# Kernel optimization log

Hardware: AMD Instinct MI355X
Metric: run time of the kernel (lower is better)

Reference implementation:

```python
import jax, jax.numpy as jnp
import numpy as np

# Config matching init_kwargs: 63 single-grapheme tokens + optional blank -> C = 64,
# trivial (identity) lexicon, ngram = 0 (no transition model), allow_repeats = True.
# Under this config the GTN composition (target chain o lexicon -> tokens graph ->
# alignments, intersected with linear emission graph, forward_score) is exactly the
# CTC forward algorithm over the extended label sequence z = [blank, y1, blank, ...,
# yL, blank], with the s-2 -> s skip allowed for ALL non-blank states (allow_repeats).

B, T, C, L = 128, 3000, 64, 128
NEG = -1e30  # effective -inf, safe in fp32


def setup_inputs() -> dict:
    key = jax.random.key(0)
    k1, k2 = jax.random.split(key)
    inputs = jax.random.normal(k1, (B, T, C), dtype=jnp.float32)  # raw logits
    # target token ids in [0, C-2]; blank = C-1 is never a target
    targets = jax.random.randint(k2, (B, L), 0, C - 1, dtype=jnp.int32)
    return {"inputs": inputs, "targets": targets}


def reference(inputs, targets):
    Bv, Tv, Cv = inputs.shape
    Lv = targets.shape[1]
    S = 2 * Lv + 1
    blank = Cv - 1
    # transitions is None -> module applies log_softmax to inputs
    logp = jax.nn.log_softmax(inputs, axis=2)  # [B, T, C]
    # extended label sequence: blanks at even positions, targets at odd positions
    z = jnp.full((Bv, S), blank, dtype=jnp.int32).at[:, 1::2].set(targets)  # [B, S]
    # per-frame emission scores for each extended state: [B, T, S] -> [T, B, S]
    em = jnp.take_along_axis(logp, jnp.broadcast_to(z[:, None, :], (Bv, Tv, S)), axis=2)
    em = jnp.transpose(em, (1, 0, 2))
    # skip transition (s-2 -> s) allowed for every non-blank (odd) state because
    # allow_repeats=True (no z[s] != z[s-2] restriction)
    skip_ok = (jnp.arange(S) % 2 == 1)  # [S]

    alpha0 = (jnp.full((Bv, S), NEG, dtype=jnp.float32)
              .at[:, 0].set(em[0, :, 0])
              .at[:, 1].set(em[0, :, 1]))

    def step(alpha, e_t):
        a1 = jnp.pad(alpha[:, :-1], ((0, 0), (1, 0)), constant_values=NEG)
        a2 = jnp.pad(alpha[:, :-2], ((0, 0), (2, 0)), constant_values=NEG)
        a2 = jnp.where(skip_ok[None, :], a2, NEG)
        new = e_t + jax.scipy.special.logsumexp(jnp.stack([alpha, a1, a2], axis=0), axis=0)
        return new, None

    alphaT, _ = jax.lax.scan(step, alpha0, em[1:])  # [B, S]
    # accepting states: last label (S-2) and trailing blank (S-1)
    ll = jax.scipy.special.logsumexp(alphaT[:, S - 2:S], axis=1)  # [B]
    # reduction='none' -> scales = 1; forward returns torch.mean over batch
    return jnp.mean(-ll)
```

## Files before the change

kernel.cpp:

```cpp
#include <hip/hip_runtime.h>
#include <stdint.h>

#define BB 128
#define TT 3000
#define CC 64
#define LL 128
#define NEGf (-1e30f)
#define LOG2E 1.4426950408889634f
#define LN2f 0.6931471805599453f
#define F 12
#define NCH 250
#define NBUF 5
#define NPH (NCH + 3)
#define LSE_BLOCKS 512

typedef float f32x2 __attribute__((ext_vector_type(2)));

__device__ __forceinline__ float fexp2(float x){ return __builtin_amdgcn_exp2f(x); }
__device__ __forceinline__ float flog2(float x){ return __builtin_amdgcn_logf(x); }
__device__ __forceinline__ float shr1_neg(float x){
    int r = __builtin_amdgcn_update_dpp(__float_as_int(NEGf), __float_as_int(x),
                                        0x138, 0xF, 0xF, false);
    return __int_as_float(r);
}
#define DPPMAXT(x,c) fmaxf((x),__int_as_float(__builtin_amdgcn_update_dpp(0,__float_as_int(x),(c),0xF,0xF,true)))
#define DPPADDT(x,c) ((x)+__int_as_float(__builtin_amdgcn_update_dpp(0,__float_as_int(x),(c),0xF,0xF,true)))
#define RED64(OP,x) { x=OP(x,0x111); x=OP(x,0x112); x=OP(x,0x114); x=OP(x,0x118); x=OP(x,0x142); x=OP(x,0x143); }

__global__ __launch_bounds__(512) void fused_kernel(const float* __restrict__ in,
                                                    const int* __restrict__ tgt,
                                                    float* __restrict__ lse,
                                                    float* __restrict__ ll2){
    __shared__ float emR[NBUF][F][132];
    __shared__ float bndR[5][3][F];
    __shared__ float laL[3008];
    __shared__ float lbL[3008];
    __shared__ float dmp[64];
    if (blockIdx.x < BB) {
        const int b = blockIdx.x;
        const int wave = threadIdx.x >> 6;
        const int lane = threadIdx.x & 63;
        const float* fb = in + (size_t)b * TT * CC;
        const uint32_t em_base  = (uint32_t)(uintptr_t)&emR[0][0][0];
        const uint32_t bnd_base = (uint32_t)(uintptr_t)&bndR[0][0][0];
        const uint32_t la_base  = (uint32_t)(uintptr_t)&laL[0];
        const uint32_t dmp_base = (uint32_t)(uintptr_t)&dmp[0];

        if (wave < 4) {
            const int w = wave;
            __builtin_amdgcn_s_setprio(1);
            if (w == 0) {
                float* bp = &bndR[0][0][0];
                if (lane < 3*F) bp[lane] = NEGf;
                if (lane < 3) bndR[lane+1][0][0] = NEGf;
                if (lane < 8) { laL[3000+lane] = NEGf; lbL[3000+lane] = 0.f; }
            }
            const bool odd = (lane & 1);
            const uint32_t em_off = odd ? (uint32_t)(32*w + (lane>>1))*4u : 512u;
            float aa = (w==0 && lane==0) ? 0.f : NEGf;
            __syncthreads();
            for (int ph = 0; ph < NPH; ++ph) {
                const int x = ph - w;
                if (x >= 0 && x < NCH) {
                    const uint32_t buf = (uint32_t)(x % NBUF);
                    const uint32_t ra  = em_base + buf*(F*132u*4u) + em_off;
                    const uint32_t xm3 = (uint32_t)(x % 3);
                    const uint32_t xp3 = (uint32_t)((x+1) % 3);
                    const uint32_t rb  = bnd_base + (uint32_t)w*144u + xm3*48u;
                    const uint32_t wbm = (lane==63) ? (bnd_base + (uint32_t)(w+1)*144u + xm3*48u)
                                                    : (dmp_base + (uint32_t)lane*4u);
                    const uint32_t wbl = (lane==63) ? (bnd_base + (uint32_t)(w+1)*144u + xp3*48u)
                                                    : (dmp_base + (uint32_t)lane*4u);
                    const uint32_t wl  = (w==3 && lane==63) ? (la_base + (uint32_t)(x*F)*4u)
                                                            : (dmp_base + (uint32_t)lane*4u);
                    float e0,e1,e2,b0,b1,b2;
                    asm volatile("ds_read_b32 %0, %1 offset:0"   : "=v"(e0) : "v"(ra));
                    asm volatile("ds_read_b32 %0, %1 offset:0"   : "=v"(b0) : "v"(rb));
                    asm volatile("ds_read_b32 %0, %1 offset:528" : "=v"(e1) : "v"(ra));
                    asm volatile("ds_read_b32 %0, %1 offset:4"   : "=v"(b1) : "v"(rb));
                    #pragma unroll
                    for (int j = 0; j < F; ++j) {
                        const int jn = (j+2 < F) ? (j+2) : (F-1);
                        asm volatile("ds_read_b32 %0, %1 offset:%2" : "=v"(e2) : "v"(ra), "n"(jn*528));
                        asm volatile("ds_read_b32 %0, %1 offset:%2" : "=v"(b2) : "v"(rb), "n"(jn*4));
                        if (j == 0)      asm volatile("s_waitcnt lgkmcnt(4)" ::: "memory");
                        else if (j == 1) asm volatile("s_waitcnt lgkmcnt(6)" ::: "memory");
                        else             asm volatile("s_waitcnt lgkmcnt(8)" ::: "memory");
                        __builtin_amdgcn_sched_barrier(0);
                        float p1 = shr1_neg(aa);
                        float p2 = shr1_neg(p1);
                        p1 = (lane==0) ? b0 : p1;
                        p2 = (lane==1) ? b0 : p2;
                        float z = odd ? p2 : NEGf;
                        float mx = fmaxf(fmaxf(aa,p1),z);
                        float md = __builtin_amdgcn_fmed3f(aa,p1,z);
                        float mn = fminf(fminf(aa,p1),z);
                        float e  = fexp2(md-mx) + fexp2(mn-mx);
                        float v  = __builtin_fmaf(e,0.5f,-0.5f);
                        float h  = __builtin_fmaf(v,0.2f,-0.25f);
                        h = __builtin_fmaf(v,h,0.33333333f);
                        h = __builtin_fmaf(v,h,-0.5f);
                        h = __builtin_fmaf(v,h,1.0f);
                        aa = __builtin_fmaf(v*h, LOG2E, mx+1.0f) + e0;
                        if (j < F-1) { asm volatile("ds_write_b32 %0, %1 offset:%2" :: "v"(wbm), "v"(aa), "n"((j+1)*4)); }
                        else         { asm volatile("ds_write_b32 %0, %1 offset:0"  :: "v"(wbl), "v"(aa)); }
                        asm volatile("ds_write_b32 %0, %1 offset:%2" :: "v"(wl), "v"(aa), "n"(j*4));
                        e0=e1; b0=b1; e1=e2; b1=b2;
                    }
                    asm volatile("s_waitcnt lgkmcnt(0)" ::: "memory");
                }
                __syncthreads();
            }
            __syncthreads();
            if (w == 0) {
                const int base = lane*47;
                float seg = 0.f;
                for (int k = 0; k < 47; ++k) seg += lbL[base+k];
                float inc = seg;
                #pragma unroll
                for (int d = 1; d < 64; d <<= 1) {
                    float t = __shfl_up(inc, d, 64);
                    if (lane >= d) inc += t;
                }
                float CBtot = __int_as_float(__builtin_amdgcn_readlane(__float_as_int(inc), 63));
                float ex = inc - seg;
                float cb = ex, gm = NEGf;
                for (int k = 0; k < 47; ++k) {
                    int idx = base+k;
                    cb += lbL[idx];
                    float g = laL[idx] + (CBtot - cb);
                    g = (idx == 2999) ? NEGf : g;
                    gm = fmaxf(gm, g);
                }
                RED64(DPPMAXT, gm);
                float gmax = __int_as_float(__builtin_amdgcn_readlane(__float_as_int(gm), 63));
                cb = ex; float se = 0.f;
                for (int k = 0; k < 47; ++k) {
                    int idx = base+k;
                    cb += lbL[idx];
                    float g = laL[idx] + (CBtot - cb);
                    g = (idx == 2999) ? NEGf : g;
                    se += fexp2(g - gmax);
                }
                RED64(DPPADDT, se);
                float S = __int_as_float(__builtin_amdgcn_readlane(__float_as_int(se), 63));
                float la256 = gmax + flog2(S);
                float la255f = laL[2999];
                float m = fmaxf(la255f, la256);
                float r = m + flog2(1.0f + fexp2(-fabsf(la255f - la256)));
                if (lane == 0) ll2[b] = r;
            }
        } else {
            const int p = wave - 4;
            const int t0 = tgt[b*LL + 2*lane];
            const int t1 = tgt[b*LL + 2*lane + 1];
            auto produce = [&](int cc) {
                const int buf = cc % NBUF;
                const float* cbase = fb + (size_t)cc * F * CC;
                float v0[3], v1[3], vb[3];
                #pragma unroll
                for (int k = 0; k < 3; ++k) {
                    const float* fr = cbase + (3*p + k)*CC;
                    v0[k] = fr[t0]; v1[k] = fr[t1]; vb[k] = fr[63];
                }
                #pragma unroll
                for (int k = 0; k < 3; ++k) {
                    const int f = 3*p + k;
                    f32x2 wv; wv.x = v0[k]*LOG2E; wv.y = v1[k]*LOG2E;
                    *(f32x2*)&emR[buf][f][2*lane] = wv;
                    if (lane == 0) {
                        float xb = vb[k]*LOG2E;
                        emR[buf][f][128] = xb;
                        lbL[cc*F + f] = xb;
                    }
                }
            };
            produce(0);
            __syncthreads();
            for (int ph = 0; ph < NPH; ++ph) {
                if (ph + 1 < NCH) produce(ph + 1);
                __syncthreads();
            }
            __syncthreads();
        }
        return;
    }
    int wv = (blockIdx.x - BB) * 8 + (threadIdx.x >> 6);
    int lane = threadIdx.x & 63;
    const int stride = LSE_BLOCKS * 8;
    for (int row = wv; row < BB * TT; row += stride) {
        float x = in[(size_t)row * CC + lane];
        float m = x;
        #pragma unroll
        for (int d = 32; d >= 1; d >>= 1) m = fmaxf(m, __shfl_xor(m, d, 64));
        float s = fexp2((x - m) * LOG2E);
        #pragma unroll
        for (int d = 32; d >= 1; d >>= 1) s += __shfl_xor(s, d, 64);
        if (lane == 0) lse[row] = m + flog2(s) * LN2f;
    }
}

__global__ __launch_bounds__(256) void bsum_kernel(const float* __restrict__ lse,
                                                   const float* __restrict__ ll2,
                                                   float* __restrict__ lossb) {
    __shared__ float red[256];
    int b = blockIdx.x;
    float s = 0.f;
    for (int i = threadIdx.x; i < TT; i += 256) s += lse[(size_t)b * TT + i];
    red[threadIdx.x] = s;
    __syncthreads();
    #pragma unroll
    for (int w = 128; w >= 1; w >>= 1) {
        if (threadIdx.x < w) red[threadIdx.x] += red[threadIdx.x + w];
        __syncthreads();
    }
    if (threadIdx.x == 0) lossb[b] = red[0] - ll2[b] * LN2f;
}

__global__ __launch_bounds__(64) void final_kernel(const float* __restrict__ lossb,
                                                   float* __restrict__ out) {
    int lane = threadIdx.x;
    float v = lossb[lane] + lossb[lane + 64];
    #pragma unroll
    for (int d = 32; d >= 1; d >>= 1) v += __shfl_xor(v, d, 64);
    if (lane == 0) out[0] = v / (float)BB;
}

extern "C" void kernel_launch(void* const* d_in, const int* in_sizes, int n_in,
                              void* d_out, int out_size, void* d_ws, size_t ws_size,
                              hipStream_t stream) {
    const float* in = (const float*)d_in[0];
    const int* tg = (const int*)d_in[1];
    float* out = (float*)d_out;
    float* lse = (float*)d_ws;
    float* ll2 = lse + (size_t)BB * TT;
    float* lossb = ll2 + BB;

    hipLaunchKernelGGL(fused_kernel, dim3(BB + LSE_BLOCKS), dim3(512), 0, stream,
                       in, tg, lse, ll2);
    hipLaunchKernelGGL(bsum_kernel, dim3(BB), dim3(256), 0, stream, lse, ll2, lossb);
    hipLaunchKernelGGL(final_kernel, dim3(1), dim3(64), 0, stream, lossb, out);
}
```

Baseline: 291.6 us.

## Batch boundary reads, defer boundary writes, and prefetch producer loads a phase ahead

The recurrence waves now read all 12 boundary values with three ds_read_b128 up front instead of per-step scalar reads. Per-step dummy writes from every lane are replaced by storing a per-step history in registers, and only lane 63 writes the boundary and laL values after the chunk. The producer waves split global loads from LDS stores so loads for chunk ph+2 are issued before the barrier, hiding global latency across a phase. This aims to cut LDS traffic and wait stalls on the serial critical path, at the cost of more registers and a short write burst at the end of each chunk.

```diff
diff --git a/kernel.cpp b/kernel.cpp
--- a/kernel.cpp
+++ b/kernel.cpp
@@ -15,6 +15,7 @@
 #define LSE_BLOCKS 512
 
 typedef float f32x2 __attribute__((ext_vector_type(2)));
+typedef float f32x4 __attribute__((ext_vector_type(4)));
 
 __device__ __forceinline__ float fexp2(float x){ return __builtin_amdgcn_exp2f(x); }
 __device__ __forceinline__ float flog2(float x){ return __builtin_amdgcn_logf(x); }
@@ -32,10 +33,9 @@
                                                     float* __restrict__ lse,
                                                     float* __restrict__ ll2){
     __shared__ float emR[NBUF][F][132];
-    __shared__ float bndR[5][3][F];
+    __shared__ __align__(16) float bndR[4][3][F];
     __shared__ float laL[3008];
     __shared__ float lbL[3008];
-    __shared__ float dmp[64];
     if (blockIdx.x < BB) {
         const int b = blockIdx.x;
         const int wave = threadIdx.x >> 6;
@@ -43,16 +43,13 @@
         const float* fb = in + (size_t)b * TT * CC;
         const uint32_t em_base  = (uint32_t)(uintptr_t)&emR[0][0][0];
         const uint32_t bnd_base = (uint32_t)(uintptr_t)&bndR[0][0][0];
-        const uint32_t la_base  = (uint32_t)(uintptr_t)&laL[0];
-        const uint32_t dmp_base = (uint32_t)(uintptr_t)&dmp[0];
 
         if (wave < 4) {
             const int w = wave;
             __builtin_amdgcn_s_setprio(1);
             if (w == 0) {
-                float* bp = &bndR[0][0][0];
-                if (lane < 3*F) bp[lane] = NEGf;
-                if (lane < 3) bndR[lane+1][0][0] = NEGf;
+                if (lane < 36) (&bndR[0][0][0])[lane] = NEGf;
+                if (lane >= 1 && lane <= 3) bndR[lane][0][0] = NEGf;
                 if (lane < 8) { laL[3000+lane] = NEGf; lbL[3000+lane] = 0.f; }
             }
             const bool odd = (lane & 1);
@@ -67,30 +64,28 @@
                     const uint32_t xm3 = (uint32_t)(x % 3);
                     const uint32_t xp3 = (uint32_t)((x+1) % 3);
                     const uint32_t rb  = bnd_base + (uint32_t)w*144u + xm3*48u;
-                    const uint32_t wbm = (lane==63) ? (bnd_base + (uint32_t)(w+1)*144u + xm3*48u)
-                                                    : (dmp_base + (uint32_t)lane*4u);
-                    const uint32_t wbl = (lane==63) ? (bnd_base + (uint32_t)(w+1)*144u + xp3*48u)
-                                                    : (dmp_base + (uint32_t)lane*4u);
-                    const uint32_t wl  = (w==3 && lane==63) ? (la_base + (uint32_t)(x*F)*4u)
-                                                            : (dmp_base + (uint32_t)lane*4u);
-                    float e0,e1,e2,b0,b1,b2;
-                    asm volatile("ds_read_b32 %0, %1 offset:0"   : "=v"(e0) : "v"(ra));
-                    asm volatile("ds_read_b32 %0, %1 offset:0"   : "=v"(b0) : "v"(rb));
-                    asm volatile("ds_read_b32 %0, %1 offset:528" : "=v"(e1) : "v"(ra));
-                    asm volatile("ds_read_b32 %0, %1 offset:4"   : "=v"(b1) : "v"(rb));
+                    f32x4 B4a, B4b, B4c; float ef[F]; float hist[F];
+                    asm volatile("ds_read_b128 %0, %1 offset:0"  : "=v"(B4a) : "v"(rb));
+                    asm volatile("ds_read_b128 %0, %1 offset:16" : "=v"(B4b) : "v"(rb));
+                    asm volatile("ds_read_b128 %0, %1 offset:32" : "=v"(B4c) : "v"(rb));
+                    asm volatile("ds_read_b32 %0, %1 offset:0"    : "=v"(ef[0]) : "v"(ra));
+                    asm volatile("ds_read_b32 %0, %1 offset:528"  : "=v"(ef[1]) : "v"(ra));
+                    asm volatile("ds_read_b32 %0, %1 offset:1056" : "=v"(ef[2]) : "v"(ra));
                     #pragma unroll
                     for (int j = 0; j < F; ++j) {
-                        const int jn = (j+2 < F) ? (j+2) : (F-1);
-                        asm volatile("ds_read_b32 %0, %1 offset:%2" : "=v"(e2) : "v"(ra), "n"(jn*528));
-                        asm volatile("ds_read_b32 %0, %1 offset:%2" : "=v"(b2) : "v"(rb), "n"(jn*4));
-                        if (j == 0)      asm volatile("s_waitcnt lgkmcnt(4)" ::: "memory");
-                        else if (j == 1) asm volatile("s_waitcnt lgkmcnt(6)" ::: "memory");
-                        else             asm volatile("s_waitcnt lgkmcnt(8)" ::: "memory");
+                        if (j + 3 < F)
+                            asm volatile("ds_read_b32 %0, %1 offset:%2"
+                                         : "=v"(ef[j+3]) : "v"(ra), "n"((j+3)*528));
+                        if (j < F-3)       asm volatile("s_waitcnt lgkmcnt(3)" ::: "memory");
+                        else if (j == F-3) asm volatile("s_waitcnt lgkmcnt(2)" ::: "memory");
+                        else if (j == F-2) asm volatile("s_waitcnt lgkmcnt(1)" ::: "memory");
+                        else               asm volatile("s_waitcnt lgkmcnt(0)" ::: "memory");
                         __builtin_amdgcn_sched_barrier(0);
+                        float bj = (j < 4) ? B4a[j & 3] : ((j < 8) ? B4b[j & 3] : B4c[j & 3]);
                         float p1 = shr1_neg(aa);
                         float p2 = shr1_neg(p1);
-                        p1 = (lane==0) ? b0 : p1;
-                        p2 = (lane==1) ? b0 : p2;
+                        p1 = (lane==0) ? bj : p1;
+                        p2 = (lane==1) ? bj : p2;
                         float z = odd ? p2 : NEGf;
                         float mx = fmaxf(fmaxf(aa,p1),z);
                         float md = __builtin_amdgcn_fmed3f(aa,p1,z);
@@ -101,11 +96,18 @@
                         h = __builtin_fmaf(v,h,0.33333333f);
                         h = __builtin_fmaf(v,h,-0.5f);
                         h = __builtin_fmaf(v,h,1.0f);
-                        aa = __builtin_fmaf(v*h, LOG2E, mx+1.0f) + e0;
-                        if (j < F-1) { asm volatile("ds_write_b32 %0, %1 offset:%2" :: "v"(wbm), "v"(aa), "n"((j+1)*4)); }
-                        else         { asm volatile("ds_write_b32 %0, %1 offset:0"  :: "v"(wbl), "v"(aa)); }
-                        asm volatile("ds_write_b32 %0, %1 offset:%2" :: "v"(wl), "v"(aa), "n"(j*4));
-                        e0=e1; b0=b1; e1=e2; b1=b2;
+                        aa = __builtin_fmaf(v*h, LOG2E, mx+1.0f) + ef[j];
+                        hist[j] = aa;
+                    }
+                    if (w < 3 && lane == 63) {
+                        float* reg = &bndR[w+1][0][0];
+                        #pragma unroll
+                        for (int j = 0; j < F-1; ++j) reg[xm3*F + j + 1] = hist[j];
+                        reg[xp3*F + 0] = hist[F-1];
+                    }
+                    if (w == 3 && lane == 63) {
+                        #pragma unroll
+                        for (int j = 0; j < F; ++j) laL[x*F + j] = hist[j];
                     }
                     asm volatile("s_waitcnt lgkmcnt(0)" ::: "memory");
                 }
@@ -154,15 +156,17 @@
             const int p = wave - 4;
             const int t0 = tgt[b*LL + 2*lane];
             const int t1 = tgt[b*LL + 2*lane + 1];
-            auto produce = [&](int cc) {
-                const int buf = cc % NBUF;
+            float v0[3], v1[3], vb[3];
+            auto loadc = [&](int cc) {
                 const float* cbase = fb + (size_t)cc * F * CC;
-                float v0[3], v1[3], vb[3];
                 #pragma unroll
                 for (int k = 0; k < 3; ++k) {
                     const float* fr = cbase + (3*p + k)*CC;
                     v0[k] = fr[t0]; v1[k] = fr[t1]; vb[k] = fr[63];
                 }
+            };
+            auto storec = [&](int cc) {
+                const int buf = cc % NBUF;
                 #pragma unroll
                 for (int k = 0; k < 3; ++k) {
                     const int f = 3*p + k;
@@ -175,10 +179,11 @@
                     }
                 }
             };
-            produce(0);
+            loadc(0); storec(0); loadc(1);
             __syncthreads();
             for (int ph = 0; ph < NPH; ++ph) {
-                if (ph + 1 < NCH) produce(ph + 1);
+                if (ph + 1 < NCH) storec(ph + 1);
+                if (ph + 2 < NCH) loadc(ph + 2);
                 __syncthreads();
             }
             __syncthreads();
```

Result: faster. 264.2 us (-9.4%).
